# Performance work log

Hardware: AMD Instinct MI355X
Metric: run time of the kernel (lower is better)

Reference implementation:

```python
import jax, jax.numpy as jnp
import numpy as np

B, C1, C2, H, W = 8, 256, 256, 64, 64
C = 256            # int(c1*e)
G = C // 16        # 16 groups (dg)
Cg = C // G        # 16 channels per group
K = 9              # 3x3 kernel sample points
BN_EPS = 1e-5

# kernel grid offsets for 3x3, dilation 1 (pad=1 centers the grid)
KH = jnp.array([-1, -1, -1, 0, 0, 0, 1, 1, 1], jnp.float32)
KW = jnp.array([-1, 0, 1, -1, 0, 1, -1, 0, 1], jnp.float32)


def setup_inputs() -> dict:
    key = jax.random.key(0)
    ks = jax.random.split(key, 10)
    x = jax.random.normal(ks[0], (B, C1, H, W), jnp.float32)
    w_cv1 = jax.random.normal(ks[1], (C, C1), jnp.float32) / np.sqrt(C1)
    b_cv1 = jax.random.normal(ks[2], (C,), jnp.float32) * 0.1
    # offset/mask linear (DCNv4 inits to zero; small scale keeps sampling sane)
    w_off = jax.random.normal(ks[3], (G * 3 * K, C), jnp.float32) * 0.01
    b_off = jax.random.normal(ks[4], (G * 3 * K,), jnp.float32) * 0.01
    w_cv2 = jax.random.normal(ks[5], (C2, C), jnp.float32) / np.sqrt(C)
    bn_gamma = jax.random.uniform(ks[6], (C2,), jnp.float32, 0.5, 1.5)
    bn_beta = jax.random.normal(ks[7], (C2,), jnp.float32) * 0.1
    bn_mean = jax.random.normal(ks[8], (C2,), jnp.float32) * 0.1
    bn_var = jax.random.uniform(ks[9], (C2,), jnp.float32, 0.5, 1.5)
    return dict(x=x, w_cv1=w_cv1, b_cv1=b_cv1, w_off=w_off, b_off=b_off,
                w_cv2=w_cv2, bn_gamma=bn_gamma, bn_beta=bn_beta,
                bn_mean=bn_mean, bn_var=bn_var)


def _gather(vflat, hi, wi):
    # vflat: (B, H*W, G, Cg); hi/wi: (B,H,W,K,G) float corner indices
    ok = ((hi >= 0) & (hi < H) & (wi >= 0) & (wi < W)).astype(vflat.dtype)
    idx = (jnp.clip(hi, 0, H - 1) * W + jnp.clip(wi, 0, W - 1)).astype(jnp.int32)
    idx = idx.reshape(B, H * W * K, G)
    idxb = jnp.broadcast_to(idx[..., None], (B, H * W * K, G, Cg))
    g = jnp.take_along_axis(vflat, idxb, axis=1)  # (B, HWK, G, Cg)
    return g.reshape(B, H, W, K, G, Cg), ok


def _dcnv4(v, off, mask):
    # v: (B,H,W,G,Cg); off: (B,H,W,G,K,2) (dh,dw); mask: (B,H,W,G,K)
    ii = jnp.arange(H, dtype=jnp.float32)
    jj = jnp.arange(W, dtype=jnp.float32)
    ph = ii[None, :, None, None, None] + KH[None, None, None, None, :] + off[..., 0]
    pw = jj[None, None, :, None, None] + KW[None, None, None, None, :] + off[..., 1]
    ph = ph.transpose(0, 1, 2, 4, 3)  # (B,H,W,K,G)
    pw = pw.transpose(0, 1, 2, 4, 3)
    h0 = jnp.floor(ph); w0 = jnp.floor(pw)
    ah = ph - h0; aw = pw - w0
    vflat = v.reshape(B, H * W, G, Cg)
    g00, ok00 = _gather(vflat, h0, w0)
    g01, ok01 = _gather(vflat, h0, w0 + 1)
    g10, ok10 = _gather(vflat, h0 + 1, w0)
    g11, ok11 = _gather(vflat, h0 + 1, w0 + 1)
    w00 = ((1 - ah) * (1 - aw) * ok00)[..., None]
    w01 = ((1 - ah) * aw * ok01)[..., None]
    w10 = (ah * (1 - aw) * ok10)[..., None]
    w11 = (ah * aw * ok11)[..., None]
    sample = w00 * g00 + w01 * g01 + w10 * g10 + w11 * g11  # (B,H,W,K,G,Cg)
    out = jnp.einsum('bhwkgc,bhwgk->bhwgc', sample, mask)
    return out.reshape(B, H, W, C).transpose(0, 3, 1, 2)  # NCHW


def reference(x, w_cv1, b_cv1, w_off, b_off, w_cv2, bn_gamma, bn_beta, bn_mean, bn_var):
    # cv1: 1x1 conv
    h1 = jnp.einsum('bchw,oc->bohw', x, w_cv1) + b_cv1[None, :, None, None]
    # offset/mask 1x1 projection, per-group layout [2K offsets, K masks]
    om = jnp.einsum('bchw,oc->bhwo', h1, w_off) + b_off
    om = om.reshape(B, H, W, G, 3 * K)
    off = om[..., :2 * K].reshape(B, H, W, G, K, 2)
    mask = om[..., 2 * K:]  # DCNv4: no softmax, used directly
    v = h1.transpose(0, 2, 3, 1).reshape(B, H, W, G, Cg)
    y = _dcnv4(v, off, mask)
    # cv2: 1x1 conv (no bias)
    y = jnp.einsum('bchw,oc->bohw', y, w_cv2)
    # BatchNorm (eval mode)
    scale = (bn_gamma / jnp.sqrt(bn_var + BN_EPS))[None, :, None, None]
    y = (y - bn_mean[None, :, None, None]) * scale + bn_beta[None, :, None, None]
    # SiLU
    return y * jax.nn.sigmoid(y)
```

## Files before the change

### kernel.cpp

```cpp
#include <hip/hip_runtime.h>

#define HW 4096
#define CCH 256
#define MOFF 432
#define PTOT 32768
#define PDIM 68
#define PIMG (PDIM*PDIM)

typedef unsigned short u16;
typedef __attribute__((ext_vector_type(8))) short short8;
typedef __attribute__((ext_vector_type(8))) unsigned short u16x8;
typedef __attribute__((ext_vector_type(4))) unsigned short u16x4;
typedef __attribute__((ext_vector_type(4))) float f32x4;

__device__ __forceinline__ u16 f2b(float f){
  unsigned int u = __float_as_uint(f);
  unsigned int rounding = 0x7FFFu + ((u >> 16) & 1u);
  return (u16)((u + rounding) >> 16);
}
__device__ __forceinline__ float b2f(u16 s){
  return __uint_as_float(((unsigned int)s) << 16);
}

__global__ __launch_bounds__(256) void k_prep(const float* __restrict__ x,
    const float* __restrict__ w1, const float* __restrict__ w2,
    const float* __restrict__ woff, const float* __restrict__ b1,
    const float* __restrict__ boff,
    const float* __restrict__ gamma, const float* __restrict__ beta,
    const float* __restrict__ mean, const float* __restrict__ var,
    u16* __restrict__ xT, u16* __restrict__ wb_big, u16* __restrict__ wb2,
    float* __restrict__ bnA, float* __restrict__ bnB,
    float* __restrict__ bcomb, u16* __restrict__ h1p){
  __shared__ float tile[64][65];
  const int r = blockIdx.x, t = threadIdx.x;
  if (r < 2048){
    const int pb = (r & 63) * 64, cb = ((r >> 6) & 3) * 64, b = r >> 8;
    const float* src = x + ((size_t)(b * CCH + cb)) * HW + pb;
    #pragma unroll
    for (int pass = 0; pass < 4; ++pass){
      int c_l = pass * 16 + (t >> 4);
      int pq = (t & 15) * 4;
      float4 v = *reinterpret_cast<const float4*>(&src[(size_t)c_l * HW + pq]);
      tile[pq + 0][c_l] = v.x; tile[pq + 1][c_l] = v.y;
      tile[pq + 2][c_l] = v.z; tile[pq + 3][c_l] = v.w;
    }
    __syncthreads();
    #pragma unroll
    for (int pass = 0; pass < 4; ++pass){
      int p_l = pass * 16 + (t >> 4);
      int cq = (t & 15) * 4;
      u16x4 o4;
      #pragma unroll
      for (int j = 0; j < 4; ++j) o4[j] = f2b(tile[p_l][cq + j]);
      *reinterpret_cast<u16x4*>(&xT[((size_t)b * HW + pb + p_l) * CCH + cb + cq]) = o4;
    }
  }
  else if (r < 2304){ int o = r - 2048; wb_big[o*256 + t] = f2b(w1[o*256 + t]); }
  else if (r < 2384){ wb_big[(688 + (r - 2304)) * 256 + t] = 0; }
  else if (r < 2640){ int o = r - 2384; wb2[o*256 + t] = f2b(w2[o*256 + t]); }
  else if (r == 2640){
    if (t < 256){
      float sc = gamma[t] * rsqrtf(var[t] + 1e-5f);
      bnA[t] = sc;
      bnB[t] = beta[t] - mean[t] * sc;
    }
  } else if (r < 3169){
    int n = (r - 2641) * 128 + (t >> 1);
    int seg = t & 1;
    int plane = n / 528, m = n % 528;
    int row, col;
    if (m < 136){ row = m / 68; col = m % 68; }
    else if (m < 272){ int mm = m - 136; row = 66 + mm / 68; col = mm % 68; }
    else { int mm = m - 272; row = 2 + (mm >> 2); int c4 = mm & 3; col = (c4 & 1) + 66 * (c4 >> 1); }
    u16x8 z = {};
    *reinterpret_cast<u16x8*>(&h1p[((size_t)plane * PIMG + row * PDIM + col) * 16 + seg * 8]) = z;
  } else {
    float* wr_ = &tile[0][0];
    float* pb  = wr_ + 256;
    const int j = r - 3169;
    wr_[t] = woff[j * 256 + t];
    __syncthreads();
    float s = 0.f;
    #pragma unroll 8
    for (int m = 0; m < 256; ++m) s += wr_[m] * w1[m * 256 + t];
    wb_big[(256 + j) * 256 + t] = f2b(s);
    pb[t] = wr_[t] * b1[t];
    __syncthreads();
    if (t == 0){
      float bs = boff[j];
      for (int m = 0; m < 256; ++m) bs += pb[m];
      bcomb[j] = bs;
    }
  }
}

__global__ __launch_bounds__(256, 2) void k_gemm_big(const u16* __restrict__ A,
    const u16* __restrict__ Bw, const float* __restrict__ b1,
    const float* __restrict__ bcomb, u16* __restrict__ h1p,
    u16* __restrict__ om){
  __shared__ __align__(16) u16 smem[34816];
  u16* As = smem;
  u16* Bs = smem + 256 * 72;

  const int bid = blockIdx.x;
  const int xcd = bid & 7, s = bid >> 3;
  const int row_local = s / 6, cblk = s % 6;
  const int tm = (row_local * 8 + xcd) * 256;
  const int tn = cblk * 128;

  const int t = threadIdx.x;
  const int lane = t & 63;
  const int wid = t >> 6;
  const int wr = wid >> 1, wc = wid & 1;

  f32x4 acc[8][4] = {};

  for (int kc = 0; kc < 256; kc += 64){
    #pragma unroll
    for (int i = 0; i < 8; ++i){
      int idx = t + i * 256;
      int row = idx >> 3, cq = idx & 7;
      *reinterpret_cast<u16x8*>(&As[row * 72 + cq * 8]) =
        *reinterpret_cast<const u16x8*>(&A[(size_t)(tm + row) * 256 + kc + cq * 8]);
    }
    #pragma unroll
    for (int i = 0; i < 4; ++i){
      int idx = t + i * 256;
      int row = idx >> 3, cq = idx & 7;
      *reinterpret_cast<u16x8*>(&Bs[row * 72 + cq * 8]) =
        *reinterpret_cast<const u16x8*>(&Bw[(size_t)(tn + row) * 256 + kc + cq * 8]);
    }
    __syncthreads();
    #pragma unroll
    for (int kk = 0; kk < 2; ++kk){
      short8 af[8], bf[4];
      #pragma unroll
      for (int m = 0; m < 8; ++m)
        af[m] = *reinterpret_cast<const short8*>(
          &As[(wr * 128 + m * 16 + (lane & 15)) * 72 + kk * 32 + (lane >> 4) * 8]);
      #pragma unroll
      for (int n = 0; n < 4; ++n)
        bf[n] = *reinterpret_cast<const short8*>(
          &Bs[(wc * 64 + n * 16 + (lane & 15)) * 72 + kk * 32 + (lane >> 4) * 8]);
      #pragma unroll
      for (int m = 0; m < 8; ++m)
        #pragma unroll
        for (int n = 0; n < 4; ++n)
          acc[m][n] = __builtin_amdgcn_mfma_f32_16x16x32_bf16(af[m], bf[n], acc[m][n], 0, 0, 0);
    }
    __syncthreads();
  }

  constexpr int CP = 136;
  u16* C_l = smem;
  #pragma unroll
  for (int n = 0; n < 4; ++n){
    int col = wc * 64 + n * 16 + (lane & 15);
    int o = tn + col;
    float bi = (o < 256) ? b1[o] : ((o - 256 < MOFF) ? bcomb[o - 256] : 0.f);
    #pragma unroll
    for (int m = 0; m < 8; ++m){
      int r0 = wr * 128 + m * 16 + ((lane >> 4) << 2);
      #pragma unroll
      for (int j = 0; j < 4; ++j)
        C_l[(r0 + j) * CP + col] = f2b(acc[m][n][j] + bi);
    }
  }
  __syncthreads();
  #pragma unroll
  for (int pass = 0; pass < 16; ++pass){
    int row = pass * 16 + (t >> 4);
    int sg = t & 15;
    int oc = tn + sg * 8;
    int p = tm + row;
    if (tn < 256){
      int bb = p >> 12, ii = (p >> 6) & 63, jj = p & 63;
      size_t dst = ((size_t)(bb * 16 + (oc >> 4)) * PIMG + (ii + 2) * PDIM + jj + 2) * 16 + (oc & 15);
      *reinterpret_cast<u16x8*>(&h1p[dst]) =
        *reinterpret_cast<const u16x8*>(&C_l[row * CP + sg * 8]);
    } else {
      int occ = oc - 256;
      if (occ + 8 <= MOFF)
        *reinterpret_cast<u16x8*>(&om[(size_t)p * MOFF + occ]) =
          *reinterpret_cast<const u16x8*>(&C_l[row * CP + sg * 8]);
    }
  }
}

__global__ __launch_bounds__(256) void k_gemm2(const u16* __restrict__ A,
    const u16* __restrict__ Bw, const float* __restrict__ bnA,
    const float* __restrict__ bnB, float* __restrict__ out){
  __shared__ __align__(16) u16 smem[(128 + 128) * 40];
  const int t = threadIdx.x;
  const int tm = blockIdx.x * 128;
  const int tn = blockIdx.y * 128;
  const int lane = t & 63;
  const int wid = t >> 6;
  const int wr = wid >> 1, wc = wid & 1;
  constexpr int BOFF = 128 * 40;

  f32x4 acc[4][4] = {};

  for (int kc = 0; kc < 256; kc += 32){
    #pragma unroll
    for (int i = 0; i < 2; ++i){
      int v = t + i * 256;
      int row = v >> 2, cq = v & 3;
      *reinterpret_cast<u16x8*>(&smem[row * 40 + cq * 8]) =
        *reinterpret_cast<const u16x8*>(&A[(size_t)(tm + row) * 256 + kc + cq * 8]);
    }
    #pragma unroll
    for (int i = 0; i < 2; ++i){
      int v = t + i * 256;
      int row = v >> 2, cq = v & 3;
      *reinterpret_cast<u16x8*>(&smem[BOFF + row * 40 + cq * 8]) =
        *reinterpret_cast<const u16x8*>(&Bw[(size_t)(tn + row) * 256 + kc + cq * 8]);
    }
    __syncthreads();
    short8 af[4], bf[4];
    #pragma unroll
    for (int m = 0; m < 4; ++m)
      af[m] = *reinterpret_cast<const short8*>(
        &smem[(wr * 64 + m * 16 + (lane & 15)) * 40 + (lane >> 4) * 8]);
    #pragma unroll
    for (int n = 0; n < 4; ++n)
      bf[n] = *reinterpret_cast<const short8*>(
        &smem[BOFF + (wc * 64 + n * 16 + (lane & 15)) * 40 + (lane >> 4) * 8]);
    #pragma unroll
    for (int m = 0; m < 4; ++m)
      #pragma unroll
      for (int n = 0; n < 4; ++n)
        acc[m][n] = __builtin_amdgcn_mfma_f32_16x16x32_bf16(af[m], bf[n], acc[m][n], 0, 0, 0);
    __syncthreads();
  }

  const int bimg = tm >> 12;
  const int ploc = tm & 4095;
  #pragma unroll
  for (int n = 0; n < 4; ++n){
    int o = tn + wc * 64 + n * 16 + (lane & 15);
    float sA = bnA[o], sB = bnB[o];
    #pragma unroll
    for (int m = 0; m < 4; ++m){
      int prow = wr * 64 + m * 16 + ((lane >> 4) << 2);
      f32x4 st;
      #pragma unroll
      for (int j = 0; j < 4; ++j){
        float y = acc[m][n][j] * sA + sB;
        st[j] = y / (1.f + expf(-y));
      }
      *reinterpret_cast<f32x4*>(&out[((size_t)(bimg * 256 + o)) * HW + ploc + prow]) = st;
    }
  }
}

__global__ __launch_bounds__(256, 4) void k_sample(const u16* __restrict__ h1p,
    const u16* __restrict__ om, u16* __restrict__ ydcn){
  __shared__ float oms[4 * MOFF];
  __shared__ float recs[5 * 576];
  const int t = threadIdx.x;
  const int pblk = blockIdx.x * 4;
  if (t < 216){
    u16x8 v = *reinterpret_cast<const u16x8*>(&om[(size_t)pblk * MOFF + t * 8]);
    float4 lo, hi;
    lo.x = b2f(v[0]); lo.y = b2f(v[1]); lo.z = b2f(v[2]); lo.w = b2f(v[3]);
    hi.x = b2f(v[4]); hi.y = b2f(v[5]); hi.z = b2f(v[6]); hi.w = b2f(v[7]);
    *reinterpret_cast<float4*>(&oms[t * 8]) = lo;
    *reinterpret_cast<float4*>(&oms[t * 8 + 4]) = hi;
  }
  __syncthreads();

  #pragma unroll
  for (int i = 0; i < 3; ++i){
    int r = t + i * 256;
    if (i < 2 || r < 64 + 512){
      int px = r / 144, rm = r % 144;
      int g = rm / 9, k = rm % 9;
      const float* ob = &oms[px * MOFF + g * 27];
      float oh = ob[2 * k], ow = ob[2 * k + 1], m = ob[18 + k];
      int hw = (pblk + px) & 4095;
      float ph = (float)((hw >> 6) + k / 3 - 1) + oh;
      float pw = (float)((hw & 63) + k % 3 - 1) + ow;
      float h0f = floorf(ph), w0f = floorf(pw);
      float ah = ph - h0f, aw = pw - w0f;
      int h0 = (int)h0f, w0 = (int)w0f;
      int hc = min(max(h0, -2), 64) + 2;
      int wc = min(max(w0, -2), 64) + 2;
      float mh1 = m * ah, mh0 = m - mh1;
      float c01 = mh0 * aw, c00 = mh0 - c01;
      float c11 = mh1 * aw, c10 = mh1 - c11;
      recs[r]            = c00;
      recs[576 + r]      = c01;
      recs[1152 + r]     = c10;
      recs[1728 + r]     = c11;
      recs[2304 + r]     = __uint_as_float((unsigned)((hc * PDIM + wc) << 5));
    }
  }
  __syncthreads();

  const int px = t >> 6;
  const int g = (t >> 2) & 15;
  const int q = t & 3;
  const int p = pblk + px;
  const int b = p >> 12;
  const int xsel = q >> 1;
  const u16* lanebase = h1p + (size_t)(b * 16 + g) * PIMG * 16 + q * 8;
  const int ri = px * 144 + g * 9;
  const float* ctp = &recs[xsel * 576 + ri];
  const float* cbp = &recs[1152 + xsel * 576 + ri];
  const float* adp = &recs[2304 + ri];

  float acc[8] = {};
  #pragma unroll
  for (int k = 0; k < 9; ++k){
    float ct = ctp[k];
    float cb = cbp[k];
    unsigned off = __float_as_uint(adp[k]);
    const u16* c0 = (const u16*)((const char*)lanebase + off);
    u16x8 tv = *reinterpret_cast<const u16x8*>(c0);
    u16x8 bv = *reinterpret_cast<const u16x8*>(c0 + PDIM * 16);
    #pragma unroll
    for (int j = 0; j < 8; ++j)
      acc[j] += ct * b2f(tv[j]) + cb * b2f(bv[j]);
  }
  #pragma unroll
  for (int j = 0; j < 8; ++j)
    acc[j] += __shfl_xor(acc[j], 2, 64);
  if (q < 2){
    u16x8 o8;
    #pragma unroll
    for (int j = 0; j < 8; ++j) o8[j] = f2b(acc[j]);
    *reinterpret_cast<u16x8*>(&ydcn[(size_t)p * 256 + g * 16 + q * 8]) = o8;
  }
}

extern "C" void kernel_launch(void* const* d_in, const int* in_sizes, int n_in,
                              void* d_out, int out_size, void* d_ws, size_t ws_size,
                              hipStream_t stream) {
  const float* x     = (const float*)d_in[0];
  const float* w1    = (const float*)d_in[1];
  const float* b1    = (const float*)d_in[2];
  const float* woff  = (const float*)d_in[3];
  const float* boff  = (const float*)d_in[4];
  const float* w2    = (const float*)d_in[5];
  const float* gamma = (const float*)d_in[6];
  const float* beta  = (const float*)d_in[7];
  const float* mean  = (const float*)d_in[8];
  const float* var   = (const float*)d_in[9];
  float* out = (float*)d_out;
  (void)in_sizes; (void)n_in; (void)out_size; (void)ws_size;

  u16* h1p    = (u16*)d_ws;
  u16* om     = h1p + (size_t)128 * PIMG * 16;
  u16* xT     = om + (size_t)PTOT * MOFF;
  u16* ydcn   = xT + (size_t)PTOT * CCH;
  u16* wb_big = ydcn + (size_t)PTOT * CCH;
  u16* wb2    = wb_big + 768 * 256;
  float* bnA  = (float*)(wb2 + 256 * 256);
  float* bnB  = bnA + 256;
  float* bcomb = bnB + 256;

  dim3 blk(256);
  k_prep<<<dim3(3601), blk, 0, stream>>>(x, w1, w2, woff, b1, boff,
                                         gamma, beta, mean, var,
                                         xT, wb_big, wb2, bnA, bnB, bcomb, h1p);
  k_gemm_big<<<dim3(768), blk, 0, stream>>>(xT, wb_big, b1, bcomb, h1p, om);
  k_sample<<<dim3(PTOT / 4), blk, 0, stream>>>(h1p, om, ydcn);
  k_gemm2<<<dim3(PTOT / 128, 2), blk, 0, stream>>>(ydcn, wb2, bnA, bnB, out);
}
```

Measured before the change: 102.2 us.

## Fuse input transpose/bf16 cast into first GEMM, drop xT buffer

After: 98.83 us. 1.03x faster.

```diff
diff --git a/kernel.cpp b/kernel.cpp
--- a/kernel.cpp
+++ b/kernel.cpp
@@ -22,50 +22,28 @@
   return __uint_as_float(((unsigned int)s) << 16);
 }
 
-__global__ __launch_bounds__(256) void k_prep(const float* __restrict__ x,
+__global__ __launch_bounds__(256) void k_prepw(
     const float* __restrict__ w1, const float* __restrict__ w2,
     const float* __restrict__ woff, const float* __restrict__ b1,
     const float* __restrict__ boff,
     const float* __restrict__ gamma, const float* __restrict__ beta,
     const float* __restrict__ mean, const float* __restrict__ var,
-    u16* __restrict__ xT, u16* __restrict__ wb_big, u16* __restrict__ wb2,
+    u16* __restrict__ wb_big, u16* __restrict__ wb2,
     float* __restrict__ bnA, float* __restrict__ bnB,
     float* __restrict__ bcomb, u16* __restrict__ h1p){
-  __shared__ float tile[64][65];
-  const int r = blockIdx.x, t = threadIdx.x;
-  if (r < 2048){
-    const int pb = (r & 63) * 64, cb = ((r >> 6) & 3) * 64, b = r >> 8;
-    const float* src = x + ((size_t)(b * CCH + cb)) * HW + pb;
-    #pragma unroll
-    for (int pass = 0; pass < 4; ++pass){
-      int c_l = pass * 16 + (t >> 4);
-      int pq = (t & 15) * 4;
-      float4 v = *reinterpret_cast<const float4*>(&src[(size_t)c_l * HW + pq]);
-      tile[pq + 0][c_l] = v.x; tile[pq + 1][c_l] = v.y;
-      tile[pq + 2][c_l] = v.z; tile[pq + 3][c_l] = v.w;
-    }
-    __syncthreads();
-    #pragma unroll
-    for (int pass = 0; pass < 4; ++pass){
-      int p_l = pass * 16 + (t >> 4);
-      int cq = (t & 15) * 4;
-      u16x4 o4;
-      #pragma unroll
-      for (int j = 0; j < 4; ++j) o4[j] = f2b(tile[p_l][cq + j]);
-      *reinterpret_cast<u16x4*>(&xT[((size_t)b * HW + pb + p_l) * CCH + cb + cq]) = o4;
-    }
-  }
-  else if (r < 2304){ int o = r - 2048; wb_big[o*256 + t] = f2b(w1[o*256 + t]); }
-  else if (r < 2384){ wb_big[(688 + (r - 2304)) * 256 + t] = 0; }
-  else if (r < 2640){ int o = r - 2384; wb2[o*256 + t] = f2b(w2[o*256 + t]); }
-  else if (r == 2640){
+  __shared__ float sbuf[512];
+  int r = blockIdx.x, t = threadIdx.x;
+  if (r < 256) wb_big[r*256 + t] = f2b(w1[r*256 + t]);
+  else if (r < 336){ wb_big[(688 + (r - 256)) * 256 + t] = 0; }
+  else if (r < 592){ int o = r - 336; wb2[o*256 + t] = f2b(w2[o*256 + t]); }
+  else if (r == 592){
     if (t < 256){
       float sc = gamma[t] * rsqrtf(var[t] + 1e-5f);
       bnA[t] = sc;
       bnB[t] = beta[t] - mean[t] * sc;
     }
-  } else if (r < 3169){
-    int n = (r - 2641) * 128 + (t >> 1);
+  } else if (r < 1121){
+    int n = (r - 593) * 128 + (t >> 1);
     int seg = t & 1;
     int plane = n / 528, m = n % 528;
     int row, col;
@@ -75,9 +53,9 @@
     u16x8 z = {};
     *reinterpret_cast<u16x8*>(&h1p[((size_t)plane * PIMG + row * PDIM + col) * 16 + seg * 8]) = z;
   } else {
-    float* wr_ = &tile[0][0];
-    float* pb  = wr_ + 256;
-    const int j = r - 3169;
+    float* wr_ = sbuf;
+    float* pb  = sbuf + 256;
+    const int j = r - 1121;
     wr_[t] = woff[j * 256 + t];
     __syncthreads();
     float s = 0.f;
@@ -94,163 +72,103 @@
   }
 }
 
-__global__ __launch_bounds__(256, 2) void k_gemm_big(const u16* __restrict__ A,
+__global__ __launch_bounds__(256, 3) void k_mega(const float* __restrict__ x,
     const u16* __restrict__ Bw, const float* __restrict__ b1,
     const float* __restrict__ bcomb, u16* __restrict__ h1p,
     u16* __restrict__ om){
-  __shared__ __align__(16) u16 smem[34816];
-  u16* As = smem;
-  u16* Bs = smem + 256 * 72;
-
-  const int bid = blockIdx.x;
-  const int xcd = bid & 7, s = bid >> 3;
-  const int row_local = s / 6, cblk = s % 6;
-  const int tm = (row_local * 8 + xcd) * 256;
-  const int tn = cblk * 128;
+  __shared__ __align__(16) u16 A_lds[64 * 260];
+  __shared__ __align__(16) u16 scr[9216];
 
   const int t = threadIdx.x;
+  const int tm = blockIdx.x * 64;
+  const int b = tm >> 12, ploc = tm & 4095;
   const int lane = t & 63;
   const int wid = t >> 6;
   const int wr = wid >> 1, wc = wid & 1;
 
-  f32x4 acc[8][4] = {};
-
-  for (int kc = 0; kc < 256; kc += 64){
-    #pragma unroll
-    for (int i = 0; i < 8; ++i){
-      int idx = t + i * 256;
-      int row = idx >> 3, cq = idx & 7;
-      *reinterpret_cast<u16x8*>(&As[row * 72 + cq * 8]) =
-        *reinterpret_cast<const u16x8*>(&A[(size_t)(tm + row) * 256 + kc + cq * 8]);
-    }
-    #pragma unroll
-    for (int i = 0; i < 4; ++i){
-      int idx = t + i * 256;
-      int row = idx >> 3, cq = idx & 7;
-      *reinterpret_cast<u16x8*>(&Bs[row * 72 + cq * 8]) =
-        *reinterpret_cast<const u16x8*>(&Bw[(size_t)(tn + row) * 256 + kc + cq * 8]);
-    }
-    __syncthreads();
-    #pragma unroll
-    for (int kk = 0; kk < 2; ++kk){
-      short8 af[8], bf[4];
-      #pragma unroll
-      for (int m = 0; m < 8; ++m)
-        af[m] = *reinterpret_cast<const short8*>(
-          &As[(wr * 128 + m * 16 + (lane & 15)) * 72 + kk * 32 + (lane >> 4) * 8]);
-      #pragma unroll
-      for (int n = 0; n < 4; ++n)
-        bf[n] = *reinterpret_cast<const short8*>(
-          &Bs[(wc * 64 + n * 16 + (lane & 15)) * 72 + kk * 32 + (lane >> 4) * 8]);
-      #pragma unroll
-      for (int m = 0; m < 8; ++m)
+  {
+    const float* xs = x + (size_t)b * 256 * HW + ploc;
+    #pragma unroll
+    for (int it = 0; it < 16; ++it){
+      int c = it * 16 + (t >> 4);
+      int p4 = (t & 15) * 4;
+      float4 v = *reinterpret_cast<const float4*>(&xs[(size_t)c * HW + p4]);
+      A_lds[(p4 + 0) * 260 + c] = f2b(v.x);
+      A_lds[(p4 + 1) * 260 + c] = f2b(v.y);
+      A_lds[(p4 + 2) * 260 + c] = f2b(v.z);
+      A_lds[(p4 + 3) * 260 + c] = f2b(v.w);
+    }
+  }
+  __syncthreads();
+
+  for (int oc6 = 0; oc6 < 6; ++oc6){
+    const int tn = oc6 * 128;
+    f32x4 acc[2][4] = {};
+
+    for (int kc = 0; kc < 256; kc += 64){
+      #pragma unroll
+      for (int i = 0; i < 4; ++i){
+        int idx = t + i * 256;
+        int row = idx >> 3, cq = idx & 7;
+        *reinterpret_cast<u16x8*>(&scr[row * 72 + cq * 8]) =
+          *reinterpret_cast<const u16x8*>(&Bw[(size_t)(tn + row) * 256 + kc + cq * 8]);
+      }
+      __syncthreads();
+      #pragma unroll
+      for (int kk = 0; kk < 2; ++kk){
+        short8 af[2], bf[4];
+        #pragma unroll
+        for (int m = 0; m < 2; ++m)
+          af[m] = *reinterpret_cast<const short8*>(
+            &A_lds[(wr * 32 + m * 16 + (lane & 15)) * 260 + kc + kk * 32 + (lane >> 4) * 8]);
         #pragma unroll
         for (int n = 0; n < 4; ++n)
-          acc[m][n] = __builtin_amdgcn_mfma_f32_16x16x32_bf16(af[m], bf[n], acc[m][n], 0, 0, 0);
-    }
-    __syncthreads();
-  }
-
-  constexpr int CP = 136;
-  u16* C_l = smem;
-  #pragma unroll
-  for (int n = 0; n < 4; ++n){
-    int col = wc * 64 + n * 16 + (lane & 15);
-    int o = tn + col;
-    float bi = (o < 256) ? b1[o] : ((o - 256 < MOFF) ? bcomb[o - 256] : 0.f);
-    #pragma unroll
-    for (int m = 0; m < 8; ++m){
-      int r0 = wr * 128 + m * 16 + ((lane >> 4) << 2);
-      #pragma unroll
-      for (int j = 0; j < 4; ++j)
-        C_l[(r0 + j) * CP + col] = f2b(acc[m][n][j] + bi);
-    }
-  }
-  __syncthreads();
-  #pragma unroll
-  for (int pass = 0; pass < 16; ++pass){
-    int row = pass * 16 + (t >> 4);
-    int sg = t & 15;
-    int oc = tn + sg * 8;
-    int p = tm + row;
-    if (tn < 256){
-      int bb = p >> 12, ii = (p >> 6) & 63, jj = p & 63;
-      size_t dst = ((size_t)(bb * 16 + (oc >> 4)) * PIMG + (ii + 2) * PDIM + jj + 2) * 16 + (oc & 15);
-      *reinterpret_cast<u16x8*>(&h1p[dst]) =
-        *reinterpret_cast<const u16x8*>(&C_l[row * CP + sg * 8]);
-    } else {
-      int occ = oc - 256;
-      if (occ + 8 <= MOFF)
-        *reinterpret_cast<u16x8*>(&om[(size_t)p * MOFF + occ]) =
+          bf[n] = *reinterpret_cast<const short8*>(
+            &scr[(wc * 64 + n * 16 + (lane & 15)) * 72 + kk * 32 + (lane >> 4) * 8]);
+        #pragma unroll
+        for (int m = 0; m < 2; ++m)
+          #pragma unroll
+          for (int n = 0; n < 4; ++n)
+            acc[m][n] = __builtin_amdgcn_mfma_f32_16x16x32_bf16(af[m], bf[n], acc[m][n], 0, 0, 0);
+      }
+      __syncthreads();
+    }
+
+    constexpr int CP = 136;
+    u16* C_l = scr;
+    #pragma unroll
+    for (int n = 0; n < 4; ++n){
+      int col = wc * 64 + n * 16 + (lane & 15);
+      int o = tn + col;
+      float bi = (o < 256) ? b1[o] : ((o - 256 < MOFF) ? bcomb[o - 256] : 0.f);
+      #pragma unroll
+      for (int m = 0; m < 2; ++m){
+        int r0 = wr * 32 + m * 16 + ((lane >> 4) << 2);
+        #pragma unroll
+        for (int j = 0; j < 4; ++j)
+          C_l[(r0 + j) * CP + col] = f2b(acc[m][n][j] + bi);
+      }
+    }
+    __syncthreads();
+    #pragma unroll
+    for (int pass = 0; pass < 4; ++pass){
+      int row = pass * 16 + (t >> 4);
+      int sg = t & 15;
+      int oc = tn + sg * 8;
+      int p = tm + row;
+      if (tn < 256){
+        int bb = p >> 12, ii = (p >> 6) & 63, jj = p & 63;
+        size_t dst = ((size_t)(bb * 16 + (oc >> 4)) * PIMG + (ii + 2) * PDIM + jj + 2) * 16 + (oc & 15);
+        *reinterpret_cast<u16x8*>(&h1p[dst]) =
           *reinterpret_cast<const u16x8*>(&C_l[row * CP + sg * 8]);
-    }
-  }
-}
-
-__global__ __launch_bounds__(256) void k_gemm2(const u16* __restrict__ A,
-    const u16* __restrict__ Bw, const float* __restrict__ bnA,
-    const float* __restrict__ bnB, float* __restrict__ out){
-  __shared__ __align__(16) u16 smem[(128 + 128) * 40];
-  const int t = threadIdx.x;
-  const int tm = blockIdx.x * 128;
-  const int tn = blockIdx.y * 128;
-  const int lane = t & 63;
-  const int wid = t >> 6;
-  const int wr = wid >> 1, wc = wid & 1;
-  constexpr int BOFF = 128 * 40;
-
-  f32x4 acc[4][4] = {};
-
-  for (int kc = 0; kc < 256; kc += 32){
-    #pragma unroll
-    for (int i = 0; i < 2; ++i){
-      int v = t + i * 256;
-      int row = v >> 2, cq = v & 3;
-      *reinterpret_cast<u16x8*>(&smem[row * 40 + cq * 8]) =
-        *reinterpret_cast<const u16x8*>(&A[(size_t)(tm + row) * 256 + kc + cq * 8]);
-    }
-    #pragma unroll
-    for (int i = 0; i < 2; ++i){
-      int v = t + i * 256;
-      int row = v >> 2, cq = v & 3;
-      *reinterpret_cast<u16x8*>(&smem[BOFF + row * 40 + cq * 8]) =
-        *reinterpret_cast<const u16x8*>(&Bw[(size_t)(tn + row) * 256 + kc + cq * 8]);
-    }
-    __syncthreads();
-    short8 af[4], bf[4];
-    #pragma unroll
-    for (int m = 0; m < 4; ++m)
-      af[m] = *reinterpret_cast<const short8*>(
-        &smem[(wr * 64 + m * 16 + (lane & 15)) * 40 + (lane >> 4) * 8]);
-    #pragma unroll
-    for (int n = 0; n < 4; ++n)
-      bf[n] = *reinterpret_cast<const short8*>(
-        &smem[BOFF + (wc * 64 + n * 16 + (lane & 15)) * 40 + (lane >> 4) * 8]);
-    #pragma unroll
-    for (int m = 0; m < 4; ++m)
-      #pragma unroll
-      for (int n = 0; n < 4; ++n)
-        acc[m][n] = __builtin_amdgcn_mfma_f32_16x16x32_bf16(af[m], bf[n], acc[m][n], 0, 0, 0);
-    __syncthreads();
-  }
-
-  const int bimg = tm >> 12;
-  const int ploc = tm & 4095;
-  #pragma unroll
-  for (int n = 0; n < 4; ++n){
-    int o = tn + wc * 64 + n * 16 + (lane & 15);
-    float sA = bnA[o], sB = bnB[o];
-    #pragma unroll
-    for (int m = 0; m < 4; ++m){
-      int prow = wr * 64 + m * 16 + ((lane >> 4) << 2);
-      f32x4 st;
-      #pragma unroll
-      for (int j = 0; j < 4; ++j){
-        float y = acc[m][n][j] * sA + sB;
-        st[j] = y / (1.f + expf(-y));
-      }
-      *reinterpret_cast<f32x4*>(&out[((size_t)(bimg * 256 + o)) * HW + ploc + prow]) = st;
-    }
+      } else {
+        int occ = oc - 256;
+        if (occ + 8 <= MOFF)
+          *reinterpret_cast<u16x8*>(&om[(size_t)p * MOFF + occ]) =
+            *reinterpret_cast<const u16x8*>(&C_l[row * CP + sg * 8]);
+      }
+    }
+    __syncthreads();
   }
 }
 
@@ -273,7 +191,7 @@
   #pragma unroll
   for (int i = 0; i < 3; ++i){
     int r = t + i * 256;
-    if (i < 2 || r < 64 + 512){
+    if (i < 2 || r < 576){
       int px = r / 144, rm = r % 144;
       int g = rm / 9, k = rm % 9;
       const float* ob = &oms[px * MOFF + g * 27];
@@ -334,6 +252,73 @@
   }
 }
 
+__global__ __launch_bounds__(256) void k_gemm2(const u16* __restrict__ A,
+    const u16* __restrict__ Bw, const float* __restrict__ bnA,
+    const float* __restrict__ bnB, float* __restrict__ out){
+  __shared__ __align__(16) u16 smem[(128 + 128) * 40];
+  const int t = threadIdx.x;
+  const int tm = blockIdx.x * 128;
+  const int tn = blockIdx.y * 128;
+  const int lane = t & 63;
+  const int wid = t >> 6;
+  const int wr = wid >> 1, wc = wid & 1;
+  constexpr int BOFF = 128 * 40;
+
+  f32x4 acc[4][4] = {};
+
+  for (int kc = 0; kc < 256; kc += 32){
+    #pragma unroll
+    for (int i = 0; i < 2; ++i){
+      int v = t + i * 256;
+      int row = v >> 2, cq = v & 3;
+      *reinterpret_cast<u16x8*>(&smem[row * 40 + cq * 8]) =
+        *reinterpret_cast<const u16x8*>(&A[(size_t)(tm + row) * 256 + kc + cq * 8]);
+    }
+    #pragma unroll
+    for (int i = 0; i < 2; ++i){
+      int v = t + i * 256;
+      int row = v >> 2, cq = v & 3;
+      *reinterpret_cast<u16x8*>(&smem[BOFF + row * 40 + cq * 8]) =
+        *reinterpret_cast<const u16x8*>(&Bw[(size_t)(tn + row) * 256 + kc + cq * 8]);
+    }
+    __syncthreads();
+    short8 af[4], bf[4];
+    #pragma unroll
+    for (int m = 0; m < 4; ++m)
+      af[m] = *reinterpret_cast<const short8*>(
+        &smem[(wr * 64 + m * 16 + (lane & 15)) * 40 + (lane >> 4) * 8]);
+    #pragma unroll
+    for (int n = 0; n < 4; ++n)
+      bf[n] = *reinterpret_cast<const short8*>(
+        &smem[BOFF + (wc * 64 + n * 16 + (lane & 15)) * 40 + (lane >> 4) * 8]);
+    #pragma unroll
+    for (int m = 0; m < 4; ++m)
+      #pragma unroll
+      for (int n = 0; n < 4; ++n)
+        acc[m][n] = __builtin_amdgcn_mfma_f32_16x16x32_bf16(af[m], bf[n], acc[m][n], 0, 0, 0);
+    __syncthreads();
+  }
+
+  const int bimg = tm >> 12;
+  const int ploc = tm & 4095;
+  #pragma unroll
+  for (int n = 0; n < 4; ++n){
+    int o = tn + wc * 64 + n * 16 + (lane & 15);
+    float sA = bnA[o], sB = bnB[o];
+    #pragma unroll
+    for (int m = 0; m < 4; ++m){
+      int prow = wr * 64 + m * 16 + ((lane >> 4) << 2);
+      f32x4 st;
+      #pragma unroll
+      for (int j = 0; j < 4; ++j){
+        float y = acc[m][n][j] * sA + sB;
+        st[j] = y / (1.f + expf(-y));
+      }
+      *reinterpret_cast<f32x4*>(&out[((size_t)(bimg * 256 + o)) * HW + ploc + prow]) = st;
+    }
+  }
+}
+
 extern "C" void kernel_launch(void* const* d_in, const int* in_sizes, int n_in,
                               void* d_out, int out_size, void* d_ws, size_t ws_size,
                               hipStream_t stream) {
@@ -352,8 +337,7 @@
 
   u16* h1p    = (u16*)d_ws;
   u16* om     = h1p + (size_t)128 * PIMG * 16;
-  u16* xT     = om + (size_t)PTOT * MOFF;
-  u16* ydcn   = xT + (size_t)PTOT * CCH;
+  u16* ydcn   = om + (size_t)PTOT * MOFF;
   u16* wb_big = ydcn + (size_t)PTOT * CCH;
   u16* wb2    = wb_big + 768 * 256;
   float* bnA  = (float*)(wb2 + 256 * 256);
@@ -361,10 +345,10 @@
   float* bcomb = bnB + 256;
 
   dim3 blk(256);
-  k_prep<<<dim3(3601), blk, 0, stream>>>(x, w1, w2, woff, b1, boff,
-                                         gamma, beta, mean, var,
-                                         xT, wb_big, wb2, bnA, bnB, bcomb, h1p);
-  k_gemm_big<<<dim3(768), blk, 0, stream>>>(xT, wb_big, b1, bcomb, h1p, om);
+  k_prepw<<<dim3(1553), blk, 0, stream>>>(w1, w2, woff, b1, boff,
+                                          gamma, beta, mean, var,
+                                          wb_big, wb2, bnA, bnB, bcomb, h1p);
+  k_mega<<<dim3(512), blk, 0, stream>>>(x, wb_big, b1, bcomb, h1p, om);
   k_sample<<<dim3(PTOT / 4), blk, 0, stream>>>(h1p, om, ydcn);
   k_gemm2<<<dim3(PTOT / 128, 2), blk, 0, stream>>>(ydcn, wb2, bnA, bnB, out);
 }
```
